# Kernel optimization log

Measured on AMD Instinct MI355X. Metric: run time of the kernel, lower is better.

## Reference

```python
import jax, jax.numpy as jnp
import numpy as np

T, B, NS, NC = 100, 4096, 12, 4
N = NS + NC  # tau dim


def setup_inputs() -> dict:
    key = jax.random.key(0)
    k1, k2, k3, k4, k5 = jax.random.split(key, 5)
    # Symmetric PD quadratic cost C = L L^T / N + I  -> well conditioned
    L = jax.random.normal(k1, (T, B, N, N), dtype=jnp.float32) * 0.1
    C = jnp.einsum('tbij,tbkj->tbik', L, L) + jnp.eye(N, dtype=jnp.float32)
    c = jax.random.normal(k2, (T, B, N), dtype=jnp.float32)
    # Linear dynamics x' = F [x;u] + f, state block near identity for stability
    F = jax.random.normal(k3, (T - 1, B, NS, N), dtype=jnp.float32) * 0.02
    A0 = jnp.concatenate([0.99 * jnp.eye(NS, dtype=jnp.float32),
                          jnp.zeros((NS, NC), jnp.float32)], axis=-1)
    F = F + A0  # broadcast over (T-1, B)
    f = jax.random.normal(k4, (T - 1, B, NS), dtype=jnp.float32) * 0.01
    x_init = jax.random.normal(k5, (B, NS), dtype=jnp.float32)
    return {"x_init": x_init, "C": C, "c": c, "F": F, "f": f}


def _lqr_solve(x_init, C, c, F, f):
    ns = x_init.shape[-1]
    # Pad dynamics to length T (terminal step has no dynamics; V starts at 0
    # so the padded zero F/f contribute nothing).
    Fp = jnp.concatenate([F, jnp.zeros_like(F[:1])], axis=0)  # [T,B,ns,n]
    fp = jnp.concatenate([f, jnp.zeros_like(f[:1])], axis=0)  # [T,B,ns]

    def bwd_step(carry, inp):
        V, v = carry                      # [B,ns,ns], [B,ns]
        Ct, ct, Ft, ft = inp
        # Q = C + F^T V F ; q = c + F^T (V f + v)
        Q = Ct + jnp.einsum('bsi,bst,btj->bij', Ft, V, Ft)
        Vf = jnp.einsum('bst,bt->bs', V, ft) + v
        q = ct + jnp.einsum('bsi,bs->bi', Ft, Vf)
        Qxx, Qxu = Q[:, :ns, :ns], Q[:, :ns, ns:]
        Qux, Quu = Q[:, ns:, :ns], Q[:, ns:, ns:]
        qx, qu = q[:, :ns], q[:, ns:]
        # Joint solve for K = -Quu^{-1} Qux, k = -Quu^{-1} qu
        Kk = -jnp.linalg.solve(Quu, jnp.concatenate([Qux, qu[..., None]], axis=-1))
        K, k = Kk[..., :ns], Kk[..., ns]
        Vn = Qxx + jnp.einsum('bij,bjk->bik', Qxu, K)
        Vn = 0.5 * (Vn + jnp.swapaxes(Vn, -1, -2))
        vn = qx + jnp.einsum('bij,bj->bi', Qxu, k)
        return (Vn, vn), (K, k)

    V0 = jnp.zeros((x_init.shape[0], ns, ns), C.dtype)
    v0 = jnp.zeros((x_init.shape[0], ns), C.dtype)
    _, (Kr, kr) = jax.lax.scan(bwd_step, (V0, v0),
                               (C[::-1], c[::-1], Fp[::-1], fp[::-1]))
    K, k = Kr[::-1], kr[::-1]  # [T,B,nc,ns], [T,B,nc]

    def fwd_step(x, inp):
        Ct, ct, Ft, ft, Kt, kt = inp
        u = jnp.einsum('bij,bj->bi', Kt, x) + kt
        tau = jnp.concatenate([x, u], axis=-1)
        cost = 0.5 * jnp.einsum('bi,bij,bj->b', tau, Ct, tau) \
               + jnp.einsum('bi,bi->b', ct, tau)
        xn = jnp.einsum('bij,bj->bi', Ft, tau) + ft
        return xn, (x, u, cost)

    _, (xs, us, costs) = jax.lax.scan(fwd_step, x_init, (C, c, Fp, fp, K, k))
    return xs, us, jnp.sum(costs, axis=0)


def reference(x_init, C, c, F, f):
    # MPC with QuadCost + LinDx and no box constraints: the iLQR loop
    # converges in one exact LQR solve (Riccati backward + forward rollout).
    x, u, objs = _lqr_solve(x_init, C, c, F, f)
    return x, u, objs
```

## Files before the change

### kernel.cpp

```cpp
#include <hip/hip_runtime.h>
#include <hip/hip_fp16.h>

#define TT 100
#define BB 4096
#define GS 488


#define FENCE() asm volatile("s_waitcnt lgkmcnt(0)" ::: "memory")

template<int CTRL>
__device__ __forceinline__ float qbcast(float x){
  return __int_as_float(__builtin_amdgcn_update_dpp(0, __float_as_int(x), CTRL, 0xF, 0xF, true));
}
__device__ __forceinline__ float quadsum(float x){
  int a = __builtin_amdgcn_update_dpp(0, __float_as_int(x), 0xB1, 0xF, 0xF, true);
  x += __int_as_float(a);
  int c = __builtin_amdgcn_update_dpp(0, __float_as_int(x), 0x4E, 0xF, 0xF, true);
  x += __int_as_float(c);
  return x;
}
__device__ __forceinline__ float readlanef(float x, int srclane){
  return __int_as_float(__builtin_amdgcn_readlane(__float_as_int(x), srclane));
}
template<int CTRL>
__device__ __forceinline__ float ror_add(float x){
  int r = __builtin_amdgcn_update_dpp(0, __float_as_int(x), CTRL, 0xF, 0xF, true);
  return x + __int_as_float(r);
}
__device__ __forceinline__ float reduce16_dpp(float x){
  x = ror_add<0x128>(x); x = ror_add<0x124>(x);
  x = ror_add<0x122>(x); x = ror_add<0x121>(x);
  return x;
}

template<int KMODE>
__device__ __forceinline__ void storeK(void* wsv, size_t of, int l, float X0,float X1,float X2,float X3){
  if (KMODE==0){
    float* wsb=(float*)wsv + of*52;
    if (l<12)       ((float4*)wsb)[l]  = make_float4(X0,X1,X2,X3);
    else if (l==12) ((float4*)wsb)[12] = make_float4(X0,X1,X2,X3);
  } else {
    __half* wsb=(__half*)wsv + of*52;
    if (l<12){
      wsb[l*4+0]=__float2half(X0); wsb[l*4+1]=__float2half(X1);
      wsb[l*4+2]=__float2half(X2); wsb[l*4+3]=__float2half(X3);
    } else if (l==12){
      wsb[48]=__float2half(X0); wsb[49]=__float2half(X1);
      wsb[50]=__float2half(X2); wsb[51]=__float2half(X3);
    }
  }
}
template<int KMODE>
__device__ __forceinline__ float4 loadKcol(const void* wsv, size_t of, int l){
  if (KMODE==0) return ((const float4*)((const float*)wsv + of*52))[l];
  const __half* p=(const __half*)wsv + of*52 + l*4;
  return make_float4(__half2float(p[0]),__half2float(p[1]),__half2float(p[2]),__half2float(p[3]));
}
template<int KMODE>
__device__ __forceinline__ float loadkk(const void* wsv, size_t of, int r){
  if (KMODE==0) return ((const float*)wsv)[of*52+48+r];
  return __half2float(((const __half*)wsv)[of*52+48+r]);
}

template<int KMODE>
__global__ __launch_bounds__(256)
void lqr_fused(const float* __restrict__ xinit,
               const float* __restrict__ Cg,
               const float* __restrict__ cg,
               const float* __restrict__ Fg,
               const float* __restrict__ fg,
               float* __restrict__ out,
               void* __restrict__ wsv)
{
  __shared__ float smem[GS*4];
  const int tid  = threadIdx.x;
  const int lane = tid & 63;
  const int wv   = tid >> 6;
  const int b    = blockIdx.x*4 + wv;
  const int l    = lane >> 2;
  const int qd   = lane & 3;

  float* __restrict__ Vb = smem + wv*GS;
  float* __restrict__ Fl = Vb + 144;
  float* __restrict__ vv = Vb + 384;
  float* __restrict__ tb = Vb + 396;

  if (l<12){
    if (qd<3) *(float4*)(Vb + l*12 + 4*qd) = make_float4(0,0,0,0);
    else vv[l]=0.f;
  }

  float4 sCq; float sc_;
  float4 sFst=make_float4(0,0,0,0); float sftv=0.f;
  {
    const size_t of = ((size_t)(TT-1)*BB + b);
    sCq = ((const float4*)(Cg + of*256 + l*16))[qd];
    sc_ = cg[of*16+l];
  }

  for (int tt=TT-1; tt>=0; --tt){
    const bool hasF = (tt < TT-1);
    const float4 Cq=sCq; const float rc=sc_;
    const float4 Fst=sFst; const float ftv=sftv;

    if (hasF){
      if (lane<48) *(float4*)(Fl + l*20 + 4*qd) = Fst;
      if (qd==0 && l<12) tb[l]=ftv;
    }
    FENCE();

    if (tt>0){
      const size_t of = ((size_t)(tt-1)*BB + b);
      sCq = ((const float4*)(Cg + of*256 + l*16))[qd];
      sc_ = cg[of*16+l];
      if (lane<48) sFst = ((const float4*)(Fg + of*192))[lane];
      if (qd==0 && l<12) sftv = fg[of*12+l];
    }

    float Qr0=Cq.x, Qr1=Cq.y, Qr2=Cq.z, Qr3=Cq.w;
    float qf=0.f;
    if (hasF){
      float Ftj[12];
      #pragma unroll
      for (int t=0;t<12;t++) Ftj[t]=Fl[t*20+l];
      const int s0=3*qd;
      float W0,W1,W2;
      {
        const float4* vr0=(const float4*)(Vb+(s0+0)*12);
        const float4* vr1=(const float4*)(Vb+(s0+1)*12);
        const float4* vr2=(const float4*)(Vb+(s0+2)*12);
        float4 a0=vr0[0],a1=vr0[1],a2=vr0[2];
        W0 = a0.x*Ftj[0]+a0.y*Ftj[1]+a0.z*Ftj[2]+a0.w*Ftj[3]
           + a1.x*Ftj[4]+a1.y*Ftj[5]+a1.z*Ftj[6]+a1.w*Ftj[7]
           + a2.x*Ftj[8]+a2.y*Ftj[9]+a2.z*Ftj[10]+a2.w*Ftj[11];
        float4 b0=vr1[0],b1=vr1[1],b2=vr1[2];
        W1 = b0.x*Ftj[0]+b0.y*Ftj[1]+b0.z*Ftj[2]+b0.w*Ftj[3]
           + b1.x*Ftj[4]+b1.y*Ftj[5]+b1.z*Ftj[6]+b1.w*Ftj[7]
           + b2.x*Ftj[8]+b2.y*Ftj[9]+b2.z*Ftj[10]+b2.w*Ftj[11];
        float4 c0=vr2[0],c1=vr2[1],c2=vr2[2];
        W2 = c0.x*Ftj[0]+c0.y*Ftj[1]+c0.z*Ftj[2]+c0.w*Ftj[3]
           + c1.x*Ftj[4]+c1.y*Ftj[5]+c1.z*Ftj[6]+c1.w*Ftj[7]
           + c2.x*Ftj[8]+c2.y*Ftj[9]+c2.z*Ftj[10]+c2.w*Ftj[11];
      }
      float Wf[12];
      Wf[0] =qbcast<0x00>(W0); Wf[1] =qbcast<0x00>(W1); Wf[2] =qbcast<0x00>(W2);
      Wf[3] =qbcast<0x55>(W0); Wf[4] =qbcast<0x55>(W1); Wf[5] =qbcast<0x55>(W2);
      Wf[6] =qbcast<0xAA>(W0); Wf[7] =qbcast<0xAA>(W1); Wf[8] =qbcast<0xAA>(W2);
      Wf[9] =qbcast<0xFF>(W0); Wf[10]=qbcast<0xFF>(W1); Wf[11]=qbcast<0xFF>(W2);
      #pragma unroll
      for (int s=0;s<12;s++){
        const float4 f4 = *(const float4*)(Fl + s*20 + 4*qd);
        Qr0 += f4.x*Wf[s]; Qr1 += f4.y*Wf[s];
        Qr2 += f4.z*Wf[s]; Qr3 += f4.w*Wf[s];
      }
      qf = W0*tb[s0] + W1*tb[s0+1] + W2*tb[s0+2];
      const float fta = qd==0?Ftj[0]:qd==1?Ftj[3]:qd==2?Ftj[6]:Ftj[9];
      const float ftb = qd==0?Ftj[1]:qd==1?Ftj[4]:qd==2?Ftj[7]:Ftj[10];
      const float ftc = qd==0?Ftj[2]:qd==1?Ftj[5]:qd==2?Ftj[8]:Ftj[11];
      qf += fta*vv[s0] + ftb*vv[s0+1] + ftc*vv[s0+2];
    }
    const float qv = rc + quadsum(qf);

    float a00=readlanef(Qr0,51),a01=readlanef(Qr0,55),a02=readlanef(Qr0,59),a03=readlanef(Qr0,63);
    float a10=readlanef(Qr1,51),a11=readlanef(Qr1,55),a12=readlanef(Qr1,59),a13=readlanef(Qr1,63);
    float a20=readlanef(Qr2,51),a21=readlanef(Qr2,55),a22=readlanef(Qr2,59),a23=readlanef(Qr2,63);
    float a30=readlanef(Qr3,51),a31=readlanef(Qr3,55),a32=readlanef(Qr3,59),a33=readlanef(Qr3,63);
    const float qu0=readlanef(qv,48),qu1=readlanef(qv,52),qu2=readlanef(qv,56),qu3=readlanef(qv,60);

    const float b0=-qbcast<0xFF>(Qr0), b1=-qbcast<0xFF>(Qr1),
                b2=-qbcast<0xFF>(Qr2), b3=-qbcast<0xFF>(Qr3);
    float bb0=b0,bb1=b1,bb2=b2,bb3=b3;

    const float i0=1.0f/a00;
    const float m10=a10*i0,m20=a20*i0,m30=a30*i0;
    a11-=m10*a01;a12-=m10*a02;a13-=m10*a03;
    a21-=m20*a01;a22-=m20*a02;a23-=m20*a03;
    a31-=m30*a01;a32-=m30*a02;a33-=m30*a03;
    bb1-=m10*bb0;bb2-=m20*bb0;bb3-=m30*bb0;
    const float i1=1.0f/a11;
    const float m21=a21*i1,m31=a31*i1;
    a22-=m21*a12;a23-=m21*a13;
    a32-=m31*a12;a33-=m31*a13;
    bb2-=m21*bb1;bb3-=m31*bb1;
    const float i2=1.0f/a22;
    const float m32=a32*i2;
    a33-=m32*a23;
    bb3-=m32*bb2;
    const float X3=bb3/a33;
    const float X2=(bb2-a23*X3)*i2;
    const float X1=(bb1-a12*X2-a13*X3)*i1;
    const float X0=(bb0-a01*X1-a02*X2-a03*X3)*i0;
    float c0=-qu0,c1=-qu1,c2=-qu2,c3=-qu3;
    c1-=m10*c0;c2-=m20*c0;c3-=m30*c0;
    c2-=m21*c1;c3-=m31*c1;
    c3-=m32*c2;
    const float k3=c3/a33;
    const float k2v=(c2-a23*k3)*i2;
    const float k1=(c1-a12*k2v-a13*k3)*i1;
    const float k0=(c0-a01*k1-a02*k2v-a03*k3)*i0;

    if (qd==0)
      storeK<KMODE>(wsv, (size_t)tt*BB+b, l,
                    l<12?X0:k0, l<12?X1:k1, l<12?X2:k2v, l<12?X3:k3);

    float vn0=Qr0, vn1=Qr1, vn2=Qr2, vn3=Qr3;
    #pragma unroll
    for (int r=0;r<4;r++){
      const float Xr = r==0?X0:r==1?X1:r==2?X2:X3;
      vn0 += __shfl(Qr0, 48+4*r+qd, 64) * Xr;
      vn1 += __shfl(Qr1, 48+4*r+qd, 64) * Xr;
      vn2 += __shfl(Qr2, 48+4*r+qd, 64) * Xr;
      vn3 += __shfl(Qr3, 48+4*r+qd, 64) * Xr;
    }
    if (l<12){
      if (qd<3){
        *(float4*)(Vb + l*12 + 4*qd) = make_float4(vn0,vn1,vn2,vn3);
      } else {
        vv[l] = qv + Qr0*k0 + Qr1*k1 + Qr2*k2v + Qr3*k3;
      }
    }
  }

  asm volatile("s_waitcnt vmcnt(0)" ::: "memory");

  const int fl = lane & 15;
  const int g4 = lane >> 4;

  float xj = (g4==0 && fl<12)? xinit[(size_t)b*12+fl] : 0.f;
  double costacc=0.0;

  float4 sCa; float sc2_;
  float4 sF0=make_float4(0,0,0,0),sF1=sF0,sF2=sF0,sF3=sF0; float sf_=0.f;
  float4 sK=make_float4(0,0,0,0); float sk_=0.f;
  {
    const float4* pc=(const float4*)(Cg + (size_t)b*256 + fl*16);
    sCa=pc[g4];
    sc2_=cg[(size_t)b*16+fl];
    if (g4==0 && fl<12){
      const float4* pf=(const float4*)(Fg + (size_t)b*192 + fl*16);
      sF0=pf[0];sF1=pf[1];sF2=pf[2];sF3=pf[3];
      sf_=fg[(size_t)b*12+fl];
      sK=loadKcol<KMODE>(wsv,(size_t)b,fl);
    }
    if (g4==0 && fl>=12) sk_=loadkk<KMODE>(wsv,(size_t)b,fl-12);
  }

  for (int t=0;t<TT;t++){
    float4 Ca=sCa; float rc=sc2_;
    float4 F0=sF0,F1=sF1,F2=sF2,F3=sF3; float rf=sf_;
    float4 K4=sK; float kl=sk_;

    if (t+1<TT){
      const size_t of=((size_t)(t+1)*BB + b);
      const float4* pc=(const float4*)(Cg + of*256 + fl*16);
      sCa=pc[g4];
      sc2_=cg[of*16+fl];
      if (g4==0 && fl<12){
        sK=loadKcol<KMODE>(wsv,of,fl);
        if (t+1<TT-1){
          const float4* pf=(const float4*)(Fg + of*192 + fl*16);
          sF0=pf[0];sF1=pf[1];sF2=pf[2];sF3=pf[3];
          sf_=fg[of*12+fl];
        }
      }
      if (g4==0 && fl>=12) sk_=loadkk<KMODE>(wsv,of,fl-12);
    }

    float pr0=0.f,pr1=0.f,pr2=0.f,pr3=0.f;
    if (g4==0 && fl<12){ pr0=K4.x*xj; pr1=K4.y*xj; pr2=K4.z*xj; pr3=K4.w*xj; }
    pr0=reduce16_dpp(pr0); pr1=reduce16_dpp(pr1);
    pr2=reduce16_dpp(pr2); pr3=reduce16_dpp(pr3);

    float* tbuf = tb + (t&1)*16;
    float tauj=0.f;
    if (g4==0){
      if (fl<12) tauj=xj;
      else {
        const float ur=(fl==12)?pr0:(fl==13)?pr1:(fl==14)?pr2:pr3;
        tauj=ur+kl;
      }
      tbuf[fl]=tauj;
    }
    FENCE();

    const float taul = tbuf[fl];
    const float4 tq = ((const float4*)tbuf)[g4];

    const float dot_p = Ca.x*tq.x + Ca.y*tq.y + Ca.z*tq.z + Ca.w*tq.w;
    costacc += (double)( taul*0.5f*dot_p + (g4==0 ? taul*rc : 0.f) );

    if (g4==0){
      if (fl<12) out[(size_t)t*BB*12 + (size_t)b*12 + fl] = xj;
      else       out[(size_t)TT*BB*12 + (size_t)t*BB*4 + (size_t)b*4 + (fl-12)] = tauj;
    }

    if (t<TT-1 && g4==0 && fl<12){
      const float4* tp=(const float4*)tbuf;
      const float4 t0=tp[0],t1=tp[1],t2=tp[2],t3=tp[3];
      xj = rf
         + F0.x*t0.x+F0.y*t0.y+F0.z*t0.z+F0.w*t0.w
         + F1.x*t1.x+F1.y*t1.y+F1.z*t1.z+F1.w*t1.w
         + F2.x*t2.x+F2.y*t2.y+F2.z*t2.z+F2.w*t2.w
         + F3.x*t3.x+F3.y*t3.y+F3.z*t3.z+F3.w*t3.w;
    }
  }

  costacc+=__shfl_xor(costacc,1,64);  costacc+=__shfl_xor(costacc,2,64);
  costacc+=__shfl_xor(costacc,4,64);  costacc+=__shfl_xor(costacc,8,64);
  costacc+=__shfl_xor(costacc,16,64); costacc+=__shfl_xor(costacc,32,64);
  if (lane==0) out[(size_t)TT*BB*16 + b]=(float)costacc;
}

extern "C" void kernel_launch(void* const* d_in, const int* in_sizes, int n_in,
                              void* d_out, int out_size, void* d_ws, size_t ws_size,
                              hipStream_t stream){
  (void)in_sizes; (void)n_in; (void)out_size;
  const float* xinit=(const float*)d_in[0];
  const float* C    =(const float*)d_in[1];
  const float* c    =(const float*)d_in[2];
  const float* F    =(const float*)d_in[3];
  const float* f    =(const float*)d_in[4];
  const size_t need_f32 = (size_t)TT*BB*52*sizeof(float);
  if (ws_size >= need_f32){
    lqr_fused<0><<<dim3(BB/4), dim3(256), 0, stream>>>(xinit,C,c,F,f,(float*)d_out,d_ws);
  } else {
    lqr_fused<1><<<dim3(BB/4), dim3(256), 0, stream>>>(xinit,C,c,F,f,(float*)d_out,d_ws);
  }
}
```

Baseline: 440.8 us.

## Process two batch elements per wavefront with interleaved ILP, fast reciprocals

```diff
diff --git a/kernel.cpp b/kernel.cpp
--- a/kernel.cpp
+++ b/kernel.cpp
@@ -7,6 +7,8 @@
 
 
 #define FENCE() asm volatile("s_waitcnt lgkmcnt(0)" ::: "memory")
+
+__device__ __forceinline__ float frcp(float x){ return __builtin_amdgcn_rcpf(x); }
 
 template<int CTRL>
 __device__ __forceinline__ float qbcast(float x){
@@ -34,13 +36,13 @@
 }
 
 template<int KMODE>
-__device__ __forceinline__ void storeK(void* wsv, size_t of, int l, float X0,float X1,float X2,float X3){
+__device__ __forceinline__ void storeK(void* wsb_, int l, float X0,float X1,float X2,float X3){
   if (KMODE==0){
-    float* wsb=(float*)wsv + of*52;
+    float* wsb=(float*)wsb_;
     if (l<12)       ((float4*)wsb)[l]  = make_float4(X0,X1,X2,X3);
     else if (l==12) ((float4*)wsb)[12] = make_float4(X0,X1,X2,X3);
   } else {
-    __half* wsb=(__half*)wsv + of*52;
+    __half* wsb=(__half*)wsb_;
     if (l<12){
       wsb[l*4+0]=__float2half(X0); wsb[l*4+1]=__float2half(X1);
       wsb[l*4+2]=__float2half(X2); wsb[l*4+3]=__float2half(X3);
@@ -51,19 +53,38 @@
   }
 }
 template<int KMODE>
-__device__ __forceinline__ float4 loadKcol(const void* wsv, size_t of, int l){
-  if (KMODE==0) return ((const float4*)((const float*)wsv + of*52))[l];
-  const __half* p=(const __half*)wsv + of*52 + l*4;
+__device__ __forceinline__ float4 loadKcol(const void* wsb_, int l){
+  if (KMODE==0) return ((const float4*)wsb_)[l];
+  const __half* p=(const __half*)wsb_ + l*4;
   return make_float4(__half2float(p[0]),__half2float(p[1]),__half2float(p[2]),__half2float(p[3]));
 }
 template<int KMODE>
-__device__ __forceinline__ float loadkk(const void* wsv, size_t of, int r){
-  if (KMODE==0) return ((const float*)wsv)[of*52+48+r];
-  return __half2float(((const __half*)wsv)[of*52+48+r]);
+__device__ __forceinline__ float loadkk(const void* wsb_, int r){
+  if (KMODE==0) return ((const float*)wsb_)[48+r];
+  return __half2float(((const __half*)wsb_)[48+r]);
+}
+
+__device__ __forceinline__ void wtrip(const float* Vb, const float* Ftj, int s0,
+                                      float& W0, float& W1, float& W2){
+  const float4* vr0=(const float4*)(Vb+(s0+0)*12);
+  const float4* vr1=(const float4*)(Vb+(s0+1)*12);
+  const float4* vr2=(const float4*)(Vb+(s0+2)*12);
+  float4 a0=vr0[0],a1=vr0[1],a2=vr0[2];
+  W0 = a0.x*Ftj[0]+a0.y*Ftj[1]+a0.z*Ftj[2]+a0.w*Ftj[3]
+     + a1.x*Ftj[4]+a1.y*Ftj[5]+a1.z*Ftj[6]+a1.w*Ftj[7]
+     + a2.x*Ftj[8]+a2.y*Ftj[9]+a2.z*Ftj[10]+a2.w*Ftj[11];
+  float4 b0=vr1[0],b1=vr1[1],b2=vr1[2];
+  W1 = b0.x*Ftj[0]+b0.y*Ftj[1]+b0.z*Ftj[2]+b0.w*Ftj[3]
+     + b1.x*Ftj[4]+b1.y*Ftj[5]+b1.z*Ftj[6]+b1.w*Ftj[7]
+     + b2.x*Ftj[8]+b2.y*Ftj[9]+b2.z*Ftj[10]+b2.w*Ftj[11];
+  float4 c0=vr2[0],c1=vr2[1],c2=vr2[2];
+  W2 = c0.x*Ftj[0]+c0.y*Ftj[1]+c0.z*Ftj[2]+c0.w*Ftj[3]
+     + c1.x*Ftj[4]+c1.y*Ftj[5]+c1.z*Ftj[6]+c1.w*Ftj[7]
+     + c2.x*Ftj[8]+c2.y*Ftj[9]+c2.z*Ftj[10]+c2.w*Ftj[11];
 }
 
 template<int KMODE>
-__global__ __launch_bounds__(256)
+__global__ __launch_bounds__(64)
 void lqr_fused(const float* __restrict__ xinit,
                const float* __restrict__ Cg,
                const float* __restrict__ cg,
@@ -72,151 +93,216 @@
                float* __restrict__ out,
                void* __restrict__ wsv)
 {
-  __shared__ float smem[GS*4];
-  const int tid  = threadIdx.x;
-  const int lane = tid & 63;
-  const int wv   = tid >> 6;
-  const int b    = blockIdx.x*4 + wv;
+  __shared__ float smem[GS*2];
+  const int lane = threadIdx.x & 63;
+  const int bA   = blockIdx.x*2;
+  const int bB   = bA + 1;
   const int l    = lane >> 2;
   const int qd   = lane & 3;
-
-  float* __restrict__ Vb = smem + wv*GS;
-  float* __restrict__ Fl = Vb + 144;
-  float* __restrict__ vv = Vb + 384;
-  float* __restrict__ tb = Vb + 396;
+  const int KSZ  = (KMODE==0?4:2);
+
+  float* __restrict__ VbA = smem;        float* __restrict__ VbB = smem + GS;
+  float* __restrict__ FlA = VbA + 144;   float* __restrict__ FlB = VbB + 144;
+  float* __restrict__ vvA = VbA + 384;   float* __restrict__ vvB = VbB + 384;
+  float* __restrict__ tbA = VbA + 396;   float* __restrict__ tbB = VbB + 396;
 
   if (l<12){
-    if (qd<3) *(float4*)(Vb + l*12 + 4*qd) = make_float4(0,0,0,0);
-    else vv[l]=0.f;
-  }
-
-  float4 sCq; float sc_;
-  float4 sFst=make_float4(0,0,0,0); float sftv=0.f;
-  {
-    const size_t of = ((size_t)(TT-1)*BB + b);
-    sCq = ((const float4*)(Cg + of*256 + l*16))[qd];
-    sc_ = cg[of*16+l];
-  }
+    if (qd<3){
+      *(float4*)(VbA + l*12 + 4*qd) = make_float4(0,0,0,0);
+      *(float4*)(VbB + l*12 + 4*qd) = make_float4(0,0,0,0);
+    } else { vvA[l]=0.f; vvB[l]=0.f; }
+  }
+
+  const size_t ofA = ((size_t)(TT-1)*BB + bA);
+  const float* pCA = Cg + ofA*256 + l*16 + 4*qd;  const float* pCB = pCA + 256;
+  const float* pcA = cg + ofA*16 + l;             const float* pcB = pcA + 16;
+  const float* pFA = Fg + ofA*192 + lane*4;       const float* pFB = pFA + 192;
+  const float* pfA = fg + ofA*12 + l;             const float* pfB = pfA + 12;
+  char*        pWA = (char*)wsv + ofA*52*KSZ;     char*        pWB = pWA + 52*KSZ;
+
+  float4 sCqA=*(const float4*)pCA, sCqB=*(const float4*)pCB;
+  float  scA_=*pcA, scB_=*pcB;
+  float4 sFstA=make_float4(0,0,0,0), sFstB=sFstA;
+  float  sftvA=0.f, sftvB=0.f;
 
   for (int tt=TT-1; tt>=0; --tt){
     const bool hasF = (tt < TT-1);
-    const float4 Cq=sCq; const float rc=sc_;
-    const float4 Fst=sFst; const float ftv=sftv;
+    const float4 CqA=sCqA, CqB=sCqB; const float rcA=scA_, rcB=scB_;
+    const float4 FstA=sFstA, FstB=sFstB; const float ftvA=sftvA, ftvB=sftvB;
 
     if (hasF){
-      if (lane<48) *(float4*)(Fl + l*20 + 4*qd) = Fst;
-      if (qd==0 && l<12) tb[l]=ftv;
+      if (lane<48){
+        *(float4*)(FlA + l*20 + 4*qd) = FstA;
+        *(float4*)(FlB + l*20 + 4*qd) = FstB;
+      }
+      if (qd==0 && l<12){ tbA[l]=ftvA; tbB[l]=ftvB; }
     }
     FENCE();
 
     if (tt>0){
-      const size_t of = ((size_t)(tt-1)*BB + b);
-      sCq = ((const float4*)(Cg + of*256 + l*16))[qd];
-      sc_ = cg[of*16+l];
-      if (lane<48) sFst = ((const float4*)(Fg + of*192))[lane];
-      if (qd==0 && l<12) sftv = fg[of*12+l];
-    }
-
-    float Qr0=Cq.x, Qr1=Cq.y, Qr2=Cq.z, Qr3=Cq.w;
-    float qf=0.f;
+      pCA -= (size_t)BB*256; pCB -= (size_t)BB*256;
+      pcA -= (size_t)BB*16;  pcB -= (size_t)BB*16;
+      sCqA = *(const float4*)pCA; sCqB = *(const float4*)pCB;
+      scA_ = *pcA;                scB_ = *pcB;
+      if (lane<48){
+        pFA -= (size_t)BB*192; pFB -= (size_t)BB*192;
+        sFstA = *(const float4*)pFA; sFstB = *(const float4*)pFB;
+      }
+      if (qd==0 && l<12){
+        pfA -= (size_t)BB*12; pfB -= (size_t)BB*12;
+        sftvA = *pfA; sftvB = *pfB;
+      }
+    }
+
+    float QrA0=CqA.x, QrA1=CqA.y, QrA2=CqA.z, QrA3=CqA.w;
+    float QrB0=CqB.x, QrB1=CqB.y, QrB2=CqB.z, QrB3=CqB.w;
+    float qfA=0.f, qfB=0.f;
+
     if (hasF){
-      float Ftj[12];
+      float FtjA[12], FtjB[12];
       #pragma unroll
-      for (int t=0;t<12;t++) Ftj[t]=Fl[t*20+l];
+      for (int t=0;t<12;t++){ FtjA[t]=FlA[t*20+l]; FtjB[t]=FlB[t*20+l]; }
       const int s0=3*qd;
-      float W0,W1,W2;
-      {
-        const float4* vr0=(const float4*)(Vb+(s0+0)*12);
-        const float4* vr1=(const float4*)(Vb+(s0+1)*12);
-        const float4* vr2=(const float4*)(Vb+(s0+2)*12);
-        float4 a0=vr0[0],a1=vr0[1],a2=vr0[2];
-        W0 = a0.x*Ftj[0]+a0.y*Ftj[1]+a0.z*Ftj[2]+a0.w*Ftj[3]
-           + a1.x*Ftj[4]+a1.y*Ftj[5]+a1.z*Ftj[6]+a1.w*Ftj[7]
-           + a2.x*Ftj[8]+a2.y*Ftj[9]+a2.z*Ftj[10]+a2.w*Ftj[11];
-        float4 b0=vr1[0],b1=vr1[1],b2=vr1[2];
-        W1 = b0.x*Ftj[0]+b0.y*Ftj[1]+b0.z*Ftj[2]+b0.w*Ftj[3]
-           + b1.x*Ftj[4]+b1.y*Ftj[5]+b1.z*Ftj[6]+b1.w*Ftj[7]
-           + b2.x*Ftj[8]+b2.y*Ftj[9]+b2.z*Ftj[10]+b2.w*Ftj[11];
-        float4 c0=vr2[0],c1=vr2[1],c2=vr2[2];
-        W2 = c0.x*Ftj[0]+c0.y*Ftj[1]+c0.z*Ftj[2]+c0.w*Ftj[3]
-           + c1.x*Ftj[4]+c1.y*Ftj[5]+c1.z*Ftj[6]+c1.w*Ftj[7]
-           + c2.x*Ftj[8]+c2.y*Ftj[9]+c2.z*Ftj[10]+c2.w*Ftj[11];
-      }
-      float Wf[12];
-      Wf[0] =qbcast<0x00>(W0); Wf[1] =qbcast<0x00>(W1); Wf[2] =qbcast<0x00>(W2);
-      Wf[3] =qbcast<0x55>(W0); Wf[4] =qbcast<0x55>(W1); Wf[5] =qbcast<0x55>(W2);
-      Wf[6] =qbcast<0xAA>(W0); Wf[7] =qbcast<0xAA>(W1); Wf[8] =qbcast<0xAA>(W2);
-      Wf[9] =qbcast<0xFF>(W0); Wf[10]=qbcast<0xFF>(W1); Wf[11]=qbcast<0xFF>(W2);
+      float WA0,WA1,WA2, WB0,WB1,WB2;
+      wtrip(VbA, FtjA, s0, WA0,WA1,WA2);
+      wtrip(VbB, FtjB, s0, WB0,WB1,WB2);
+
+      float WfA[12], WfB[12];
+      WfA[0]=qbcast<0x00>(WA0); WfA[1]=qbcast<0x00>(WA1); WfA[2]=qbcast<0x00>(WA2);
+      WfA[3]=qbcast<0x55>(WA0); WfA[4]=qbcast<0x55>(WA1); WfA[5]=qbcast<0x55>(WA2);
+      WfA[6]=qbcast<0xAA>(WA0); WfA[7]=qbcast<0xAA>(WA1); WfA[8]=qbcast<0xAA>(WA2);
+      WfA[9]=qbcast<0xFF>(WA0); WfA[10]=qbcast<0xFF>(WA1); WfA[11]=qbcast<0xFF>(WA2);
+      WfB[0]=qbcast<0x00>(WB0); WfB[1]=qbcast<0x00>(WB1); WfB[2]=qbcast<0x00>(WB2);
+      WfB[3]=qbcast<0x55>(WB0); WfB[4]=qbcast<0x55>(WB1); WfB[5]=qbcast<0x55>(WB2);
+      WfB[6]=qbcast<0xAA>(WB0); WfB[7]=qbcast<0xAA>(WB1); WfB[8]=qbcast<0xAA>(WB2);
+      WfB[9]=qbcast<0xFF>(WB0); WfB[10]=qbcast<0xFF>(WB1); WfB[11]=qbcast<0xFF>(WB2);
+
       #pragma unroll
       for (int s=0;s<12;s++){
-        const float4 f4 = *(const float4*)(Fl + s*20 + 4*qd);
-        Qr0 += f4.x*Wf[s]; Qr1 += f4.y*Wf[s];
-        Qr2 += f4.z*Wf[s]; Qr3 += f4.w*Wf[s];
-      }
-      qf = W0*tb[s0] + W1*tb[s0+1] + W2*tb[s0+2];
-      const float fta = qd==0?Ftj[0]:qd==1?Ftj[3]:qd==2?Ftj[6]:Ftj[9];
-      const float ftb = qd==0?Ftj[1]:qd==1?Ftj[4]:qd==2?Ftj[7]:Ftj[10];
-      const float ftc = qd==0?Ftj[2]:qd==1?Ftj[5]:qd==2?Ftj[8]:Ftj[11];
-      qf += fta*vv[s0] + ftb*vv[s0+1] + ftc*vv[s0+2];
-    }
-    const float qv = rc + quadsum(qf);
-
-    float a00=readlanef(Qr0,51),a01=readlanef(Qr0,55),a02=readlanef(Qr0,59),a03=readlanef(Qr0,63);
-    float a10=readlanef(Qr1,51),a11=readlanef(Qr1,55),a12=readlanef(Qr1,59),a13=readlanef(Qr1,63);
-    float a20=readlanef(Qr2,51),a21=readlanef(Qr2,55),a22=readlanef(Qr2,59),a23=readlanef(Qr2,63);
-    float a30=readlanef(Qr3,51),a31=readlanef(Qr3,55),a32=readlanef(Qr3,59),a33=readlanef(Qr3,63);
-    const float qu0=readlanef(qv,48),qu1=readlanef(qv,52),qu2=readlanef(qv,56),qu3=readlanef(qv,60);
-
-    const float b0=-qbcast<0xFF>(Qr0), b1=-qbcast<0xFF>(Qr1),
-                b2=-qbcast<0xFF>(Qr2), b3=-qbcast<0xFF>(Qr3);
-    float bb0=b0,bb1=b1,bb2=b2,bb3=b3;
-
-    const float i0=1.0f/a00;
-    const float m10=a10*i0,m20=a20*i0,m30=a30*i0;
-    a11-=m10*a01;a12-=m10*a02;a13-=m10*a03;
-    a21-=m20*a01;a22-=m20*a02;a23-=m20*a03;
-    a31-=m30*a01;a32-=m30*a02;a33-=m30*a03;
-    bb1-=m10*bb0;bb2-=m20*bb0;bb3-=m30*bb0;
-    const float i1=1.0f/a11;
-    const float m21=a21*i1,m31=a31*i1;
-    a22-=m21*a12;a23-=m21*a13;
-    a32-=m31*a12;a33-=m31*a13;
-    bb2-=m21*bb1;bb3-=m31*bb1;
-    const float i2=1.0f/a22;
-    const float m32=a32*i2;
-    a33-=m32*a23;
-    bb3-=m32*bb2;
-    const float X3=bb3/a33;
-    const float X2=(bb2-a23*X3)*i2;
-    const float X1=(bb1-a12*X2-a13*X3)*i1;
-    const float X0=(bb0-a01*X1-a02*X2-a03*X3)*i0;
-    float c0=-qu0,c1=-qu1,c2=-qu2,c3=-qu3;
-    c1-=m10*c0;c2-=m20*c0;c3-=m30*c0;
-    c2-=m21*c1;c3-=m31*c1;
-    c3-=m32*c2;
-    const float k3=c3/a33;
-    const float k2v=(c2-a23*k3)*i2;
-    const float k1=(c1-a12*k2v-a13*k3)*i1;
-    const float k0=(c0-a01*k1-a02*k2v-a03*k3)*i0;
-
-    if (qd==0)
-      storeK<KMODE>(wsv, (size_t)tt*BB+b, l,
-                    l<12?X0:k0, l<12?X1:k1, l<12?X2:k2v, l<12?X3:k3);
-
-    float vn0=Qr0, vn1=Qr1, vn2=Qr2, vn3=Qr3;
+        const float4 f4A = *(const float4*)(FlA + s*20 + 4*qd);
+        const float4 f4B = *(const float4*)(FlB + s*20 + 4*qd);
+        QrA0 += f4A.x*WfA[s]; QrA1 += f4A.y*WfA[s];
+        QrA2 += f4A.z*WfA[s]; QrA3 += f4A.w*WfA[s];
+        QrB0 += f4B.x*WfB[s]; QrB1 += f4B.y*WfB[s];
+        QrB2 += f4B.z*WfB[s]; QrB3 += f4B.w*WfB[s];
+      }
+      qfA = WA0*tbA[s0] + WA1*tbA[s0+1] + WA2*tbA[s0+2];
+      qfB = WB0*tbB[s0] + WB1*tbB[s0+1] + WB2*tbB[s0+2];
+      const float ftaA = qd==0?FtjA[0]:qd==1?FtjA[3]:qd==2?FtjA[6]:FtjA[9];
+      const float ftbA = qd==0?FtjA[1]:qd==1?FtjA[4]:qd==2?FtjA[7]:FtjA[10];
+      const float ftcA = qd==0?FtjA[2]:qd==1?FtjA[5]:qd==2?FtjA[8]:FtjA[11];
+      qfA += ftaA*vvA[s0] + ftbA*vvA[s0+1] + ftcA*vvA[s0+2];
+      const float ftaB = qd==0?FtjB[0]:qd==1?FtjB[3]:qd==2?FtjB[6]:FtjB[9];
+      const float ftbB = qd==0?FtjB[1]:qd==1?FtjB[4]:qd==2?FtjB[7]:FtjB[10];
+      const float ftcB = qd==0?FtjB[2]:qd==1?FtjB[5]:qd==2?FtjB[8]:FtjB[11];
+      qfB += ftaB*vvB[s0] + ftbB*vvB[s0+1] + ftcB*vvB[s0+2];
+    }
+    const float qvA = rcA + quadsum(qfA);
+    const float qvB = rcB + quadsum(qfB);
+
+    float aA00=readlanef(QrA0,51),aA01=readlanef(QrA0,55),aA02=readlanef(QrA0,59),aA03=readlanef(QrA0,63);
+    float aA10=readlanef(QrA1,51),aA11=readlanef(QrA1,55),aA12=readlanef(QrA1,59),aA13=readlanef(QrA1,63);
+    float aA20=readlanef(QrA2,51),aA21=readlanef(QrA2,55),aA22=readlanef(QrA2,59),aA23=readlanef(QrA2,63);
+    float aA30=readlanef(QrA3,51),aA31=readlanef(QrA3,55),aA32=readlanef(QrA3,59),aA33=readlanef(QrA3,63);
+    const float quA0=readlanef(qvA,48),quA1=readlanef(qvA,52),quA2=readlanef(qvA,56),quA3=readlanef(qvA,60);
+    float aB00=readlanef(QrB0,51),aB01=readlanef(QrB0,55),aB02=readlanef(QrB0,59),aB03=readlanef(QrB0,63);
+    float aB10=readlanef(QrB1,51),aB11=readlanef(QrB1,55),aB12=readlanef(QrB1,59),aB13=readlanef(QrB1,63);
+    float aB20=readlanef(QrB2,51),aB21=readlanef(QrB2,55),aB22=readlanef(QrB2,59),aB23=readlanef(QrB2,63);
+    float aB30=readlanef(QrB3,51),aB31=readlanef(QrB3,55),aB32=readlanef(QrB3,59),aB33=readlanef(QrB3,63);
+    const float quB0=readlanef(qvB,48),quB1=readlanef(qvB,52),quB2=readlanef(qvB,56),quB3=readlanef(qvB,60);
+
+    const float bA0=-qbcast<0xFF>(QrA0), bA1=-qbcast<0xFF>(QrA1),
+                bA2=-qbcast<0xFF>(QrA2), bA3=-qbcast<0xFF>(QrA3);
+    const float bB0=-qbcast<0xFF>(QrB0), bB1=-qbcast<0xFF>(QrB1),
+                bB2=-qbcast<0xFF>(QrB2), bB3=-qbcast<0xFF>(QrB3);
+    float bbA0=bA0,bbA1=bA1,bbA2=bA2,bbA3=bA3;
+    float bbB0=bB0,bbB1=bB1,bbB2=bB2,bbB3=bB3;
+
+    const float iA0=frcp(aA00);
+    const float mA10=aA10*iA0,mA20=aA20*iA0,mA30=aA30*iA0;
+    aA11-=mA10*aA01;aA12-=mA10*aA02;aA13-=mA10*aA03;
+    aA21-=mA20*aA01;aA22-=mA20*aA02;aA23-=mA20*aA03;
+    aA31-=mA30*aA01;aA32-=mA30*aA02;aA33-=mA30*aA03;
+    bbA1-=mA10*bbA0;bbA2-=mA20*bbA0;bbA3-=mA30*bbA0;
+    const float iA1=frcp(aA11);
+    const float mA21=aA21*iA1,mA31=aA31*iA1;
+    aA22-=mA21*aA12;aA23-=mA21*aA13;
+    aA32-=mA31*aA12;aA33-=mA31*aA13;
+    bbA2-=mA21*bbA1;bbA3-=mA31*bbA1;
+    const float iA2=frcp(aA22);
+    const float mA32=aA32*iA2;
+    aA33-=mA32*aA23;
+    bbA3-=mA32*bbA2;
+    const float iA3=frcp(aA33);
+    const float XA3=bbA3*iA3;
+    const float XA2=(bbA2-aA23*XA3)*iA2;
+    const float XA1=(bbA1-aA12*XA2-aA13*XA3)*iA1;
+    const float XA0=(bbA0-aA01*XA1-aA02*XA2-aA03*XA3)*iA0;
+    float cA0=-quA0,cA1=-quA1,cA2=-quA2,cA3=-quA3;
+    cA1-=mA10*cA0;cA2-=mA20*cA0;cA3-=mA30*cA0;
+    cA2-=mA21*cA1;cA3-=mA31*cA1;
+    cA3-=mA32*cA2;
+    const float kA3=cA3*iA3;
+    const float kA2=(cA2-aA23*kA3)*iA2;
+    const float kA1=(cA1-aA12*kA2-aA13*kA3)*iA1;
+    const float kA0=(cA0-aA01*kA1-aA02*kA2-aA03*kA3)*iA0;
+    const float iB0=frcp(aB00);
+    const float mB10=aB10*iB0,mB20=aB20*iB0,mB30=aB30*iB0;
+    aB11-=mB10*aB01;aB12-=mB10*aB02;aB13-=mB10*aB03;
+    aB21-=mB20*aB01;aB22-=mB20*aB02;aB23-=mB20*aB03;
+    aB31-=mB30*aB01;aB32-=mB30*aB02;aB33-=mB30*aB03;
+    bbB1-=mB10*bbB0;bbB2-=mB20*bbB0;bbB3-=mB30*bbB0;
+    const float iB1=frcp(aB11);
+    const float mB21=aB21*iB1,mB31=aB31*iB1;
+    aB22-=mB21*aB12;aB23-=mB21*aB13;
+    aB32-=mB31*aB12;aB33-=mB31*aB13;
+    bbB2-=mB21*bbB1;bbB3-=mB31*bbB1;
+    const float iB2=frcp(aB22);
+    const float mB32=aB32*iB2;
+    aB33-=mB32*aB23;
+    bbB3-=mB32*bbB2;
+    const float iB3=frcp(aB33);
+    const float XB3=bbB3*iB3;
+    const float XB2=(bbB2-aB23*XB3)*iB2;
+    const float XB1=(bbB1-aB12*XB2-aB13*XB3)*iB1;
+    const float XB0=(bbB0-aB01*XB1-aB02*XB2-aB03*XB3)*iB0;
+    float cB0=-quB0,cB1=-quB1,cB2=-quB2,cB3=-quB3;
+    cB1-=mB10*cB0;cB2-=mB20*cB0;cB3-=mB30*cB0;
+    cB2-=mB21*cB1;cB3-=mB31*cB1;
+    cB3-=mB32*cB2;
+    const float kB3=cB3*iB3;
+    const float kB2=(cB2-aB23*kB3)*iB2;
+    const float kB1=(cB1-aB12*kB2-aB13*kB3)*iB1;
+    const float kB0=(cB0-aB01*kB1-aB02*kB2-aB03*kB3)*iB0;
+
+    if (qd==0){
+      storeK<KMODE>(pWA, l, l<12?XA0:kA0, l<12?XA1:kA1, l<12?XA2:kA2, l<12?XA3:kA3);
+      storeK<KMODE>(pWB, l, l<12?XB0:kB0, l<12?XB1:kB1, l<12?XB2:kB2, l<12?XB3:kB3);
+    }
+    pWA -= (size_t)BB*52*KSZ; pWB -= (size_t)BB*52*KSZ;
+
+    float vnA0=QrA0, vnA1=QrA1, vnA2=QrA2, vnA3=QrA3;
+    float vnB0=QrB0, vnB1=QrB1, vnB2=QrB2, vnB3=QrB3;
     #pragma unroll
     for (int r=0;r<4;r++){
-      const float Xr = r==0?X0:r==1?X1:r==2?X2:X3;
-      vn0 += __shfl(Qr0, 48+4*r+qd, 64) * Xr;
-      vn1 += __shfl(Qr1, 48+4*r+qd, 64) * Xr;
-      vn2 += __shfl(Qr2, 48+4*r+qd, 64) * Xr;
-      vn3 += __shfl(Qr3, 48+4*r+qd, 64) * Xr;
+      const float XrA = r==0?XA0:r==1?XA1:r==2?XA2:XA3;
+      const float XrB = r==0?XB0:r==1?XB1:r==2?XB2:XB3;
+      vnA0 += __shfl(QrA0, 48+4*r+qd, 64) * XrA;
+      vnA1 += __shfl(QrA1, 48+4*r+qd, 64) * XrA;
+      vnA2 += __shfl(QrA2, 48+4*r+qd, 64) * XrA;
+      vnA3 += __shfl(QrA3, 48+4*r+qd, 64) * XrA;
+      vnB0 += __shfl(QrB0, 48+4*r+qd, 64) * XrB;
+      vnB1 += __shfl(QrB1, 48+4*r+qd, 64) * XrB;
+      vnB2 += __shfl(QrB2, 48+4*r+qd, 64) * XrB;
+      vnB3 += __shfl(QrB3, 48+4*r+qd, 64) * XrB;
     }
     if (l<12){
       if (qd<3){
-        *(float4*)(Vb + l*12 + 4*qd) = make_float4(vn0,vn1,vn2,vn3);
+        *(float4*)(VbA + l*12 + 4*qd) = make_float4(vnA0,vnA1,vnA2,vnA3);
+        *(float4*)(VbB + l*12 + 4*qd) = make_float4(vnB0,vnB1,vnB2,vnB3);
       } else {
-        vv[l] = qv + Qr0*k0 + Qr1*k1 + Qr2*k2v + Qr3*k3;
+        vvA[l] = qvA + QrA0*kA0 + QrA1*kA1 + QrA2*kA2 + QrA3*kA3;
+        vvB[l] = qvB + QrB0*kB0 + QrB1*kB1 + QrB2*kB2 + QrB3*kB3;
       }
     }
   }
@@ -226,89 +312,131 @@
   const int fl = lane & 15;
   const int g4 = lane >> 4;
 
-  float xj = (g4==0 && fl<12)? xinit[(size_t)b*12+fl] : 0.f;
-  double costacc=0.0;
-
-  float4 sCa; float sc2_;
-  float4 sF0=make_float4(0,0,0,0),sF1=sF0,sF2=sF0,sF3=sF0; float sf_=0.f;
-  float4 sK=make_float4(0,0,0,0); float sk_=0.f;
+  float xjA = (g4==0 && fl<12)? xinit[(size_t)bA*12+fl] : 0.f;
+  float xjB = (g4==0 && fl<12)? xinit[(size_t)bB*12+fl] : 0.f;
+  double costA=0.0, costB=0.0;
+
+  const float* qCA = Cg + (size_t)bA*256 + fl*16 + 4*g4;  const float* qCB = qCA + 256;
+  const float* qcA = cg + (size_t)bA*16 + fl;             const float* qcB = qcA + 16;
+  const float* qFA = Fg + (size_t)bA*192 + fl*16;         const float* qFB = qFA + 192;
+  const float* qfA2= fg + (size_t)bA*12 + fl;             const float* qfB2= qfA2 + 12;
+  const char*  qKA = (const char*)wsv + (size_t)bA*52*KSZ; const char* qKB = qKA + 52*KSZ;
+
+  float4 sCaA, sCaB; float sc2A, sc2B;
+  float4 sFA0=make_float4(0,0,0,0),sFA1=sFA0,sFA2=sFA0,sFA3=sFA0; float sfA_=0.f;
+  float4 sFB0=sFA0,sFB1=sFA0,sFB2=sFA0,sFB3=sFA0;                 float sfB_=0.f;
+  float4 sKA=make_float4(0,0,0,0), sKB=sKA; float skA_=0.f, skB_=0.f;
   {
-    const float4* pc=(const float4*)(Cg + (size_t)b*256 + fl*16);
-    sCa=pc[g4];
-    sc2_=cg[(size_t)b*16+fl];
+    sCaA = *(const float4*)qCA;  sCaB = *(const float4*)qCB;
+    sc2A = *qcA;                 sc2B = *qcB;
     if (g4==0 && fl<12){
-      const float4* pf=(const float4*)(Fg + (size_t)b*192 + fl*16);
-      sF0=pf[0];sF1=pf[1];sF2=pf[2];sF3=pf[3];
-      sf_=fg[(size_t)b*12+fl];
-      sK=loadKcol<KMODE>(wsv,(size_t)b,fl);
-    }
-    if (g4==0 && fl>=12) sk_=loadkk<KMODE>(wsv,(size_t)b,fl-12);
+      const float4* p4A=(const float4*)qFA; const float4* p4B=(const float4*)qFB;
+      sFA0=p4A[0];sFA1=p4A[1];sFA2=p4A[2];sFA3=p4A[3];
+      sFB0=p4B[0];sFB1=p4B[1];sFB2=p4B[2];sFB3=p4B[3];
+      sfA_=*qfA2; sfB_=*qfB2;
+      sKA=loadKcol<KMODE>(qKA,fl); sKB=loadKcol<KMODE>(qKB,fl);
+    }
+    if (g4==0 && fl>=12){ skA_=loadkk<KMODE>(qKA,fl-12); skB_=loadkk<KMODE>(qKB,fl-12); }
   }
 
   for (int t=0;t<TT;t++){
-    float4 Ca=sCa; float rc=sc2_;
-    float4 F0=sF0,F1=sF1,F2=sF2,F3=sF3; float rf=sf_;
-    float4 K4=sK; float kl=sk_;
+    float4 CaA=sCaA, CaB=sCaB; float rcA=sc2A, rcB=sc2B;
+    float4 FA0=sFA0,FA1=sFA1,FA2=sFA2,FA3=sFA3; float rfA=sfA_;
+    float4 FB0=sFB0,FB1=sFB1,FB2=sFB2,FB3=sFB3; float rfB=sfB_;
+    float4 KA4=sKA, KB4=sKB; float klA=skA_, klB=skB_;
 
     if (t+1<TT){
-      const size_t of=((size_t)(t+1)*BB + b);
-      const float4* pc=(const float4*)(Cg + of*256 + fl*16);
-      sCa=pc[g4];
-      sc2_=cg[of*16+fl];
+      qCA += (size_t)BB*256; qCB += (size_t)BB*256;
+      qcA += (size_t)BB*16;  qcB += (size_t)BB*16;
+      qKA += (size_t)BB*52*KSZ; qKB += (size_t)BB*52*KSZ;
+      sCaA = *(const float4*)qCA; sCaB = *(const float4*)qCB;
+      sc2A = *qcA;                sc2B = *qcB;
       if (g4==0 && fl<12){
-        sK=loadKcol<KMODE>(wsv,of,fl);
+        sKA=loadKcol<KMODE>(qKA,fl); sKB=loadKcol<KMODE>(qKB,fl);
         if (t+1<TT-1){
-          const float4* pf=(const float4*)(Fg + of*192 + fl*16);
-          sF0=pf[0];sF1=pf[1];sF2=pf[2];sF3=pf[3];
-          sf_=fg[of*12+fl];
+          qFA += (size_t)BB*192; qFB += (size_t)BB*192;
+          qfA2 += (size_t)BB*12; qfB2 += (size_t)BB*12;
+          const float4* p4A=(const float4*)qFA; const float4* p4B=(const float4*)qFB;
+          sFA0=p4A[0];sFA1=p4A[1];sFA2=p4A[2];sFA3=p4A[3];
+          sFB0=p4B[0];sFB1=p4B[1];sFB2=p4B[2];sFB3=p4B[3];
+          sfA_=*qfA2; sfB_=*qfB2;
         }
       }
-      if (g4==0 && fl>=12) sk_=loadkk<KMODE>(wsv,of,fl-12);
-    }
-
-    float pr0=0.f,pr1=0.f,pr2=0.f,pr3=0.f;
-    if (g4==0 && fl<12){ pr0=K4.x*xj; pr1=K4.y*xj; pr2=K4.z*xj; pr3=K4.w*xj; }
-    pr0=reduce16_dpp(pr0); pr1=reduce16_dpp(pr1);
-    pr2=reduce16_dpp(pr2); pr3=reduce16_dpp(pr3);
-
-    float* tbuf = tb + (t&1)*16;
-    float tauj=0.f;
+      if (g4==0 && fl>=12){ skA_=loadkk<KMODE>(qKA,fl-12); skB_=loadkk<KMODE>(qKB,fl-12); }
+    }
+
+    float pA0=0.f,pA1=0.f,pA2=0.f,pA3=0.f, pB0=0.f,pB1=0.f,pB2=0.f,pB3=0.f;
+    if (g4==0 && fl<12){
+      pA0=KA4.x*xjA; pA1=KA4.y*xjA; pA2=KA4.z*xjA; pA3=KA4.w*xjA;
+      pB0=KB4.x*xjB; pB1=KB4.y*xjB; pB2=KB4.z*xjB; pB3=KB4.w*xjB;
+    }
+    pA0=reduce16_dpp(pA0); pA1=reduce16_dpp(pA1);
+    pA2=reduce16_dpp(pA2); pA3=reduce16_dpp(pA3);
+    pB0=reduce16_dpp(pB0); pB1=reduce16_dpp(pB1);
+    pB2=reduce16_dpp(pB2); pB3=reduce16_dpp(pB3);
+
+    float* tbufA = tbA + (t&1)*16;
+    float* tbufB = tbB + (t&1)*16;
+    float tauA=0.f, tauB=0.f;
     if (g4==0){
-      if (fl<12) tauj=xj;
+      if (fl<12){ tauA=xjA; tauB=xjB; }
       else {
-        const float ur=(fl==12)?pr0:(fl==13)?pr1:(fl==14)?pr2:pr3;
-        tauj=ur+kl;
-      }
-      tbuf[fl]=tauj;
+        const float uA=(fl==12)?pA0:(fl==13)?pA1:(fl==14)?pA2:pA3;
+        const float uB=(fl==12)?pB0:(fl==13)?pB1:(fl==14)?pB2:pB3;
+        tauA=uA+klA; tauB=uB+klB;
+      }
+      tbufA[fl]=tauA; tbufB[fl]=tauB;
     }
     FENCE();
 
-    const float taul = tbuf[fl];
-    const float4 tq = ((const float4*)tbuf)[g4];
-
-    const float dot_p = Ca.x*tq.x + Ca.y*tq.y + Ca.z*tq.z + Ca.w*tq.w;
-    costacc += (double)( taul*0.5f*dot_p + (g4==0 ? taul*rc : 0.f) );
+    const float taulA = tbufA[fl];
+    const float taulB = tbufB[fl];
+    const float4 tqA = ((const float4*)tbufA)[g4];
+    const float4 tqB = ((const float4*)tbufB)[g4];
+
+    const float dotA = CaA.x*tqA.x + CaA.y*tqA.y + CaA.z*tqA.z + CaA.w*tqA.w;
+    const float dotB = CaB.x*tqB.x + CaB.y*tqB.y + CaB.z*tqB.z + CaB.w*tqB.w;
+    costA += (double)( taulA*0.5f*dotA + (g4==0 ? taulA*rcA : 0.f) );
+    costB += (double)( taulB*0.5f*dotB + (g4==0 ? taulB*rcB : 0.f) );
 
     if (g4==0){
-      if (fl<12) out[(size_t)t*BB*12 + (size_t)b*12 + fl] = xj;
-      else       out[(size_t)TT*BB*12 + (size_t)t*BB*4 + (size_t)b*4 + (fl-12)] = tauj;
+      if (fl<12){
+        out[(size_t)t*BB*12 + (size_t)bA*12 + fl] = xjA;
+        out[(size_t)t*BB*12 + (size_t)bB*12 + fl] = xjB;
+      } else {
+        out[(size_t)TT*BB*12 + (size_t)t*BB*4 + (size_t)bA*4 + (fl-12)] = tauA;
+        out[(size_t)TT*BB*12 + (size_t)t*BB*4 + (size_t)bB*4 + (fl-12)] = tauB;
+      }
     }
 
     if (t<TT-1 && g4==0 && fl<12){
-      const float4* tp=(const float4*)tbuf;
-      const float4 t0=tp[0],t1=tp[1],t2=tp[2],t3=tp[3];
-      xj = rf
-         + F0.x*t0.x+F0.y*t0.y+F0.z*t0.z+F0.w*t0.w
-         + F1.x*t1.x+F1.y*t1.y+F1.z*t1.z+F1.w*t1.w
-         + F2.x*t2.x+F2.y*t2.y+F2.z*t2.z+F2.w*t2.w
-         + F3.x*t3.x+F3.y*t3.y+F3.z*t3.z+F3.w*t3.w;
-    }
-  }
-
-  costacc+=__shfl_xor(costacc,1,64);  costacc+=__shfl_xor(costacc,2,64);
-  costacc+=__shfl_xor(costacc,4,64);  costacc+=__shfl_xor(costacc,8,64);
-  costacc+=__shfl_xor(costacc,16,64); costacc+=__shfl_xor(costacc,32,64);
-  if (lane==0) out[(size_t)TT*BB*16 + b]=(float)costacc;
+      const float4* tpA=(const float4*)tbufA;
+      const float4* tpB=(const float4*)tbufB;
+      const float4 a0=tpA[0],a1=tpA[1],a2=tpA[2],a3=tpA[3];
+      const float4 b0=tpB[0],b1=tpB[1],b2=tpB[2],b3=tpB[3];
+      xjA = rfA
+        + FA0.x*a0.x+FA0.y*a0.y+FA0.z*a0.z+FA0.w*a0.w
+        + FA1.x*a1.x+FA1.y*a1.y+FA1.z*a1.z+FA1.w*a1.w
+        + FA2.x*a2.x+FA2.y*a2.y+FA2.z*a2.z+FA2.w*a2.w
+        + FA3.x*a3.x+FA3.y*a3.y+FA3.z*a3.z+FA3.w*a3.w;
+      xjB = rfB
+        + FB0.x*b0.x+FB0.y*b0.y+FB0.z*b0.z+FB0.w*b0.w
+        + FB1.x*b1.x+FB1.y*b1.y+FB1.z*b1.z+FB1.w*b1.w
+        + FB2.x*b2.x+FB2.y*b2.y+FB2.z*b2.z+FB2.w*b2.w
+        + FB3.x*b3.x+FB3.y*b3.y+FB3.z*b3.z+FB3.w*b3.w;
+    }
+  }
+
+  costA+=__shfl_xor(costA,1,64);  costA+=__shfl_xor(costA,2,64);
+  costA+=__shfl_xor(costA,4,64);  costA+=__shfl_xor(costA,8,64);
+  costA+=__shfl_xor(costA,16,64); costA+=__shfl_xor(costA,32,64);
+  costB+=__shfl_xor(costB,1,64);  costB+=__shfl_xor(costB,2,64);
+  costB+=__shfl_xor(costB,4,64);  costB+=__shfl_xor(costB,8,64);
+  costB+=__shfl_xor(costB,16,64); costB+=__shfl_xor(costB,32,64);
+  if (lane==0){
+    out[(size_t)TT*BB*16 + bA]=(float)costA;
+    out[(size_t)TT*BB*16 + bB]=(float)costB;
+  }
 }
 
 extern "C" void kernel_launch(void* const* d_in, const int* in_sizes, int n_in,
@@ -322,8 +450,8 @@
   const float* f    =(const float*)d_in[4];
   const size_t need_f32 = (size_t)TT*BB*52*sizeof(float);
   if (ws_size >= need_f32){
-    lqr_fused<0><<<dim3(BB/4), dim3(256), 0, stream>>>(xinit,C,c,F,f,(float*)d_out,d_ws);
+    lqr_fused<0><<<dim3(BB/2), dim3(64), 0, stream>>>(xinit,C,c,F,f,(float*)d_out,d_ws);
   } else {
-    lqr_fused<1><<<dim3(BB/4), dim3(256), 0, stream>>>(xinit,C,c,F,f,(float*)d_out,d_ws);
-  }
-}
+    lqr_fused<1><<<dim3(BB/2), dim3(64), 0, stream>>>(xinit,C,c,F,f,(float*)d_out,d_ws);
+  }
+}
```

Result: slower. 508.8 us (+15.4%).
